# Optimization experiments

Hardware: AMD Instinct MI355X
Metric: run time of the kernel (lower is better)

Reference implementation:

```python
import jax, jax.numpy as jnp
import numpy as np

N = 100000   # nodes
E = 1600000  # edges
IN = 128     # input feature dim
C = 64       # per-layer output dim (filters)
H = 2        # attention heads
EPS = 1e-5   # batchnorm eps


def setup_inputs() -> dict:
    key = jax.random.key(0)
    ks = jax.random.split(key, 32)
    rn = lambda k, s, sc=0.05: jax.random.normal(k, s, jnp.float32) * sc
    inp = {
        "x": jax.random.normal(ks[0], (N, IN), jnp.float32),
        "edge_index": jax.random.randint(ks[1], (2, E), 0, N, jnp.int32),
        # GATConv layer 0 (IN -> C, H heads, concat=False)
        "W0": rn(ks[2], (IN, H * C)), "as0": rn(ks[3], (H, C)), "ad0": rn(ks[4], (H, C)), "b0": jnp.zeros((C,), jnp.float32),
        "skip0": rn(ks[5], (IN, C)),  # Linear(IN->C, bias=False); layers 1,2 skips are Identity
        "g0": jnp.ones((C,), jnp.float32), "be0": jnp.zeros((C,), jnp.float32),
        # GATConv layer 1 (C -> C)
        "W1": rn(ks[6], (C, H * C)), "as1": rn(ks[7], (H, C)), "ad1": rn(ks[8], (H, C)), "b1": jnp.zeros((C,), jnp.float32),
        "g1": jnp.ones((C,), jnp.float32), "be1": jnp.zeros((C,), jnp.float32),
        # GATConv layer 2 (C -> C)
        "W2": rn(ks[9], (C, H * C)), "as2": rn(ks[10], (H, C)), "ad2": rn(ks[11], (H, C)), "b2": jnp.zeros((C,), jnp.float32),
        "g2": jnp.ones((C,), jnp.float32), "be2": jnp.zeros((C,), jnp.float32),
        # JK projection for input (IN -> C, with bias); other projections are Identity
        "projW": rn(ks[12], (IN, C)), "projb": jnp.zeros((C,), jnp.float32),
    }
    return inp


def _gat(x, edge_index, W, a_src, a_dst, b):
    # PyG GATConv, concat=False: mean over heads, bias added after mean.
    h = (x @ W).reshape(-1, H, C)                 # [N, H, C]
    src, dst = edge_index[0], edge_index[1]
    e_src = jnp.sum(h * a_src, axis=-1)           # [N, H]
    e_dst = jnp.sum(h * a_dst, axis=-1)           # [N, H]
    e = jax.nn.leaky_relu(e_src[src] + e_dst[dst], 0.2)  # [E, H]
    m = jax.ops.segment_max(e, dst, num_segments=N)      # neighbor softmax (stable)
    w = jnp.exp(e - m[dst])
    denom = jax.ops.segment_sum(w, dst, num_segments=N)
    alpha = w / (denom[dst] + 1e-16)              # [E, H]
    out = jax.ops.segment_sum(alpha[:, :, None] * h[src], dst, num_segments=N)  # [N, H, C]
    return out.mean(axis=1) + b


def _bn(x, g, b):
    # BatchNorm1d, training-mode batch statistics (deterministic reference)
    mu = x.mean(axis=0)
    var = x.var(axis=0)
    return (x - mu) * jax.lax.rsqrt(var + EPS) * g + b


def reference(x, edge_index, W0, as0, ad0, b0, skip0, g0, be0,
              W1, as1, ad1, b1, g1, be1,
              W2, as2, ad2, b2, g2, be2,
              projW, projb):
    lrelu = lambda v: jax.nn.leaky_relu(v, 0.01)  # nn.LeakyReLU default
    jk0 = x @ projW + projb                       # proj_lyrs[0]
    # layer 0: GAT + projected skip, BN, (dropout=identity in eval), LeakyReLU
    h1 = _gat(x, edge_index, W0, as0, ad0, b0) + x @ skip0
    h1 = lrelu(_bn(h1, g0, be0))
    # layer 1: identity skip
    h2 = _gat(h1, edge_index, W1, as1, ad1, b1) + h1
    h2 = lrelu(_bn(h2, g1, be1))
    # layer 2: identity skip
    h3 = _gat(h2, edge_index, W2, as2, ad2, b2) + h2
    h3 = lrelu(_bn(h3, g2, be2))
    # jumping knowledge, mode='max': elementwise max over [input_proj, h1, h2, h3]
    return jnp.max(jnp.stack([jk0, h1, h2, h3], axis=0), axis=0)
```

## Files before the change

### kernel.cpp

```cpp
#include <hip/hip_runtime.h>

#define NN 100000
#define NE 1600000

constexpr int NBUC = 196;
constexpr int BIN_CHUNK = 4096;
constexpr int NB_BIN = (NE + BIN_CHUNK - 1) / BIN_CHUNK;
constexpr int ACHUNK = 16;

typedef __attribute__((ext_vector_type(8))) short s16x8;
typedef __attribute__((ext_vector_type(4))) float f32x4;
typedef __attribute__((ext_vector_type(2))) float f32x2;

template <int M>
struct IC {
    static constexpr int value = M;
};

__device__ inline unsigned short f2bf(float f) {
    unsigned int u = __float_as_uint(f);
    return (unsigned short)((u + 0x7fffu + ((u >> 16) & 1u)) >> 16);
}
__device__ inline float bf_lo(unsigned int pk) { return __uint_as_float(pk << 16); }
__device__ inline float bf_hi(unsigned int pk) { return __uint_as_float(pk & 0xffff0000u); }
__device__ inline float h2f(unsigned int u) {
    _Float16 h;
    unsigned short s = (unsigned short)u;
    __builtin_memcpy(&h, &s, 2);
    return (float)h;
}

__global__ void zero_u32(unsigned int* p, int n) {
    int i = blockIdx.x * blockDim.x + threadIdx.x;
    if (i < n) p[i] = 0u;
}

__global__ __launch_bounds__(256) void bucket_count(const int* __restrict__ dst,
                                                    int* __restrict__ bcount) {
    __shared__ int hist[NBUC];
    int t = threadIdx.x;
    for (int b = t; b < NBUC; b += 256) hist[b] = 0;
    __syncthreads();
    int beg = blockIdx.x * BIN_CHUNK;
    int end = min(beg + BIN_CHUNK, NE);
    for (int i = beg + t; i < end; i += 256) atomicAdd(&hist[dst[i] >> 9], 1);
    __syncthreads();
    for (int b = t; b < NBUC; b += 256)
        if (hist[b]) atomicAdd(&bcount[b], hist[b]);
}

__global__ void bucket_scan(const int* __restrict__ bcount, int* __restrict__ bbase,
                            int* __restrict__ bucket_cursor, int* __restrict__ offsets) {
    if (threadIdx.x == 0) {
        int run = 0;
        for (int b = 0; b < NBUC; ++b) {
            bbase[b] = run;
            bucket_cursor[b] = run;
            run += bcount[b];
        }
        bbase[NBUC] = NE;
        offsets[NN] = NE;
    }
}

__global__ __launch_bounds__(256) void bin_edges(const int* __restrict__ src,
                                                 const int* __restrict__ dst,
                                                 int* __restrict__ bucket_cursor,
                                                 unsigned int* __restrict__ binned) {
    __shared__ int hist[NBUC];
    __shared__ int base[NBUC];
    int t = threadIdx.x;
    for (int b = t; b < NBUC; b += 256) hist[b] = 0;
    __syncthreads();
    int beg = blockIdx.x * BIN_CHUNK;
    int end = min(beg + BIN_CHUNK, NE);
    for (int i = beg + t; i < end; i += 256) atomicAdd(&hist[dst[i] >> 9], 1);
    __syncthreads();
    for (int b = t; b < NBUC; b += 256) {
        base[b] = hist[b] ? atomicAdd(&bucket_cursor[b], hist[b]) : 0;
        hist[b] = 0;
    }
    __syncthreads();
    for (int i = beg + t; i < end; i += 256) {
        int d = dst[i];
        int bk = d >> 9;
        int loc = atomicAdd(&hist[bk], 1);
        binned[base[bk] + loc] = ((unsigned)(d & 511) << 17) | (unsigned)src[i];
    }
}

__global__ __launch_bounds__(256) void bucket_sort(const unsigned int* __restrict__ binned,
                                                   const int* __restrict__ bbase,
                                                   int* __restrict__ offsets,
                                                   int* __restrict__ csr_src,
                                                   int* __restrict__ csr_dst) {
    __shared__ int deg[512];
    __shared__ int loc[512];
    __shared__ int s2[256];
    int t = threadIdx.x;
    int b = blockIdx.x;
    int beg = bbase[b], end = bbase[b + 1];
    int nbase = b << 9;
    deg[t] = 0;
    deg[t + 256] = 0;
    __syncthreads();
    for (int i = beg + t; i < end; i += 256) atomicAdd(&deg[binned[i] >> 17], 1);
    __syncthreads();
    int pairsum = deg[2 * t] + deg[2 * t + 1];
    s2[t] = pairsum;
    __syncthreads();
    for (int off = 1; off < 256; off <<= 1) {
        int v = (t >= off) ? s2[t - off] : 0;
        __syncthreads();
        s2[t] += v;
        __syncthreads();
    }
    int ex = s2[t] - pairsum;
    loc[2 * t] = ex;
    loc[2 * t + 1] = ex + deg[2 * t];
    __syncthreads();
    for (int i = t; i < 512; i += 256) {
        int node = nbase + i;
        if (node < NN) offsets[node] = beg + loc[i];
    }
    __syncthreads();
    for (int i = beg + t; i < end; i += 256) {
        unsigned int v = binned[i];
        int dl = v >> 17;
        int pos = atomicAdd(&loc[dl], 1);
        csr_src[beg + pos] = (int)(v & 0x1FFFFu);
        csr_dst[beg + pos] = nbase + dl;
    }
}

__global__ void prep_weights(const float* __restrict__ W0, const float* __restrict__ skip0,
                             const float* __restrict__ projW, const float* __restrict__ W1,
                             const float* __restrict__ W2,
                             const float* __restrict__ as0, const float* __restrict__ ad0,
                             const float* __restrict__ as1, const float* __restrict__ ad1,
                             const float* __restrict__ as2, const float* __restrict__ ad2,
                             unsigned short* __restrict__ Wtcat,
                             unsigned short* __restrict__ Wt1,
                             unsigned short* __restrict__ Wt2) {
    int i = blockIdx.x * 256 + threadIdx.x;
    if (i < 16384) {
        int oc = i >> 7, k = i & 127;
        Wtcat[oc * 128 + k] = f2bf(W0[k * 128 + oc]);
    } else if (i < 32768) {
        int j = i - 16384;
        int oc = j >> 7, k = j & 127;
        float v = (oc < 64) ? skip0[k * 64 + oc] : projW[k * 64 + (oc - 64)];
        Wtcat[132 * 128 + oc * 128 + k] = f2bf(v);
    } else if (i < 40960) {
        int j = i - 32768, oc = j >> 6, k = j & 63;
        Wt1[oc * 64 + k] = f2bf(W1[k * 128 + oc]);
    } else if (i < 49152) {
        int j = i - 40960, oc = j >> 6, k = j & 63;
        Wt2[oc * 64 + k] = f2bf(W2[k * 128 + oc]);
    } else if (i < 50688) {
        int e = i - 49152;
        if (e < 512) {
            int k = e >> 2, sc = e & 3, head = sc & 1;
            const float* av = (sc < 2 ? as0 : ad0) + head * 64;
            const float* wr = W0 + k * 128 + head * 64;
            float s = 0.f;
            for (int c = 0; c < 64; ++c) s += wr[c] * av[c];
            Wtcat[(128 + sc) * 128 + k] = f2bf(s);
        } else if (e < 1024) {
            int j = e - 512, k = j >> 2, sc = j & 3;
            Wtcat[132 * 128 + (128 + sc) * 128 + k] = 0;
        } else if (e < 1280) {
            int j = e - 1024, k = j >> 2, sc = j & 3, head = sc & 1;
            const float* av = (sc < 2 ? as1 : ad1) + head * 64;
            const float* wr = W1 + k * 128 + head * 64;
            float s = 0.f;
            for (int c = 0; c < 64; ++c) s += wr[c] * av[c];
            Wt1[(128 + sc) * 64 + k] = f2bf(s);
        } else {
            int j = e - 1280, k = j >> 2, sc = j & 3, head = sc & 1;
            const float* av = (sc < 2 ? as2 : ad2) + head * 64;
            const float* wr = W2 + k * 128 + head * 64;
            float s = 0.f;
            for (int c = 0; c < 64; ++c) s += wr[c] * av[c];
            Wt2[(128 + sc) * 64 + k] = f2bf(s);
        }
    }
}

template <int K, bool L0, bool XFORM>
__global__ __launch_bounds__(256, 4) void gemm_mfma(
    const void* __restrict__ Xv, const unsigned short* __restrict__ Wt,
    unsigned int* __restrict__ Hq32, _Float16* __restrict__ skipx,
    _Float16* __restrict__ jkproj, const float* __restrict__ projb,
    const float* __restrict__ bnsc,
    unsigned int* __restrict__ e_srcpk, unsigned int* __restrict__ e_dstpk) {
    constexpr int KP = K + 8;
    constexpr int NC = 132;
    __shared__ unsigned short Bs[NC * KP];
    int t = threadIdx.x;
    int tile = L0 ? blockIdx.x : 0;
    int rbase = (L0 ? blockIdx.y : blockIdx.x) * 64;
    const unsigned short* Wtg = Wt + (size_t)tile * NC * K;

    for (int i = t; i < NC * (K / 8); i += 256) {
        int oc = i / (K / 8);
        int k8 = (i % (K / 8)) * 8;
        uint4 v = *(const uint4*)&Wtg[(size_t)oc * K + k8];
        *(uint4*)&Bs[oc * KP + k8] = v;
    }

    int lane = t & 63, wv = t >> 6;
    int lr = lane & 15, quad = lane >> 4;
    int arow = wv * 16 + lr;
    int grow = rbase + arow;
    bool rowok = grow < NN;

    s16x8 afrag[K / 32];
#pragma unroll
    for (int ks = 0; ks < K / 32; ++ks) {
        int kq = ks * 32 + quad * 8;
        float v[8];
        if (rowok) {
            if constexpr (!XFORM) {
                const float* Xf = (const float*)Xv;
                float4 p0 = *(const float4*)&Xf[(size_t)grow * K + kq];
                float4 p1 = *(const float4*)&Xf[(size_t)grow * K + kq + 4];
                v[0] = p0.x; v[1] = p0.y; v[2] = p0.z; v[3] = p0.w;
                v[4] = p1.x; v[5] = p1.y; v[6] = p1.z; v[7] = p1.w;
            } else {
                const _Float16* Xh = (const _Float16*)Xv;
                uint4 rw = *(const uint4*)&Xh[(size_t)grow * K + kq];
                unsigned rr[4] = {rw.x, rw.y, rw.z, rw.w};
#pragma unroll
                for (int q = 0; q < 4; ++q) {
                    v[2 * q] = h2f(rr[q]);
                    v[2 * q + 1] = h2f(rr[q] >> 16);
                }
#pragma unroll
                for (int c = 0; c < 8; ++c) {
                    float val = v[c] * bnsc[kq + c] + bnsc[64 + kq + c];
                    v[c] = val >= 0.f ? val : 0.01f * val;
                }
            }
        } else {
#pragma unroll
            for (int c = 0; c < 8; ++c) v[c] = 0.f;
        }
        unsigned short* ap = (unsigned short*)&afrag[ks];
#pragma unroll
        for (int c = 0; c < 8; ++c) ap[c] = f2bf(v[c]);
    }
    __syncthreads();

    f32x4 acc[8];
    f32x4 acc8 = (f32x4)(0.f);
#pragma unroll
    for (int c = 0; c < 8; ++c) acc[c] = (f32x4)(0.f);
#pragma unroll
    for (int ks = 0; ks < K / 32; ++ks) {
        s16x8 a = afrag[ks];
        int k0 = ks * 32;
#pragma unroll
        for (int ct = 0; ct < 8; ++ct) {
            s16x8 b = *(const s16x8*)&Bs[(ct * 16 + lr) * KP + k0 + quad * 8];
            acc[ct] = __builtin_amdgcn_mfma_f32_16x16x32_bf16(a, b, acc[ct], 0, 0, 0);
        }
        s16x8 b9 = *(const s16x8*)&Bs[(128 + (lr & 3)) * KP + k0 + quad * 8];
        acc8 = __builtin_amdgcn_mfma_f32_16x16x32_bf16(a, b9, acc8, 0, 0, 0);
    }

    bool hblock = (!L0) || (tile == 0);
#pragma unroll
    for (int reg = 0; reg < 4; ++reg) {
        int row = rbase + wv * 16 + quad * 4 + reg;
        if (hblock) {
            if (row < NN) {
#pragma unroll
                for (int ct = 0; ct < 4; ++ct) {
                    int pk = __builtin_amdgcn_cvt_pk_fp8_f32(acc[ct][reg], acc[ct + 4][reg],
                                                             0, false);
                    int pn = __shfl_xor(pk, 1, 64);
                    if (!(lr & 1))
                        Hq32[(size_t)row * 32 + ct * 8 + (lr >> 1)] =
                            (unsigned int)((pk & 0xFFFF) | (pn << 16));
                }
            }
            float own = acc8[reg];
            float par = __shfl_xor(own, 1, 64);
            if (row < NN) {
                unsigned int pkv = (unsigned)f2bf(own) | ((unsigned)f2bf(par) << 16);
                if (lr == 0) e_srcpk[row] = pkv;
                else if (lr == 2) e_dstpk[row] = pkv;
            }
        } else if (row < NN) {
#pragma unroll
            for (int ct = 0; ct < 4; ++ct)
                skipx[(size_t)row * 64 + ct * 16 + lr] = (_Float16)acc[ct][reg];
#pragma unroll
            for (int ct = 4; ct < 8; ++ct) {
                int c = (ct - 4) * 16 + lr;
                jkproj[(size_t)row * 64 + c] = (_Float16)(acc[ct][reg] + projb[c]);
            }
        }
    }
}

__global__ void edge_w(const int* __restrict__ csr_src, const int* __restrict__ csr_dst,
                       const unsigned int* __restrict__ e_srcpk,
                       const unsigned int* __restrict__ e_dstpk,
                       uint2* __restrict__ erec) {
    int i = blockIdx.x * blockDim.x + threadIdx.x;
    if (i >= NE) return;
    int s = csr_src[i];
    unsigned int q = e_srcpk[s];
    unsigned int r = e_dstpk[csr_dst[i]];
    float a0 = bf_lo(q) + bf_lo(r);
    float a1 = bf_hi(q) + bf_hi(r);
    a0 = a0 >= 0.f ? a0 : 0.2f * a0;
    a1 = a1 >= 0.f ? a1 : 0.2f * a1;
    unsigned int w = (unsigned int)f2bf(__expf(a0)) | ((unsigned int)f2bf(__expf(a1)) << 16);
    erec[i] = make_uint2((unsigned)s, w);
}

__global__ __launch_bounds__(256) void aggregate(
    const int* __restrict__ offsets, const uint2* __restrict__ erec,
    const unsigned int* __restrict__ Hq32, const _Float16* __restrict__ skipsrc,
    const float* __restrict__ bnsc, const float* __restrict__ bias,
    _Float16* __restrict__ hraw) {
    int wave = threadIdx.x >> 6;
    int lane = threadIdx.x & 63;
    int w = blockIdx.x * 4 + wave;
    int n0 = w * ACHUNK;
    if (n0 >= NN) return;
    int n1 = min(n0 + ACHUNK, NN);
    const unsigned char* __restrict__ Hq8 = (const unsigned char*)Hq32;
    int voff = lane * 2;

    float bsc = 0.f, bsh = 0.f;
    if (bnsc) {
        bsc = bnsc[lane];
        bsh = bnsc[64 + lane];
    }
    float bi = bias[lane];

    int end = __builtin_amdgcn_readfirstlane(offsets[n0]);
    for (int n = n0; n < n1; ++n) {
        int beg = end;
        end = __builtin_amdgcn_readfirstlane(offsets[n + 1]);
        float a0 = 0.f, a1 = 0.f, den0 = 0.f, den1 = 0.f;
        int j = beg;

        auto batch = [&](auto Mc) {
            constexpr int M = decltype(Mc)::value;
            uint2 ee[M];
#pragma unroll
            for (int u = 0; u < M; ++u) ee[u] = erec[j + u];
            int ss[M];
            unsigned ww[M];
#pragma unroll
            for (int u = 0; u < M; ++u) {
                ss[u] = __builtin_amdgcn_readfirstlane((int)ee[u].x);
                ww[u] = (unsigned)__builtin_amdgcn_readfirstlane((int)ee[u].y);
            }
            unsigned short uu[M];
#pragma unroll
            for (int u = 0; u < M; ++u)
                uu[u] = *(const unsigned short*)(Hq8 + (size_t)ss[u] * 128 + voff);
#pragma unroll
            for (int u = 0; u < M; ++u) {
                float w0 = bf_lo(ww[u]), w1 = bf_hi(ww[u]);
                f32x2 hv = __builtin_amdgcn_cvt_pk_f32_fp8((int)uu[u], false);
                den0 += w0;
                den1 += w1;
                a0 += w0 * hv[0];
                a1 += w1 * hv[1];
            }
            j += M;
        };

        while (j + 16 <= end) batch(IC<16>{});
        if (j + 8 <= end) batch(IC<8>{});
        if (j + 4 <= end) batch(IC<4>{});
        if (j + 2 <= end) batch(IC<2>{});
        if (j < end) batch(IC<1>{});

        float sv = (float)skipsrc[(size_t)n * 64 + lane];
        if (bnsc) {
            sv = sv * bsc + bsh;
            sv = sv >= 0.f ? sv : 0.01f * sv;
        }
        float id0 = 1.f / (den0 + 1e-16f), id1 = 1.f / (den1 + 1e-16f);
        float o = 0.5f * (a0 * id0 + a1 * id1) + bi + sv;
        hraw[(size_t)n * 64 + lane] = (_Float16)o;
    }
}

__global__ void bn_stats(const _Float16* __restrict__ x, float* __restrict__ sums) {
    __shared__ float ls[256], ls2[256];
    int t = threadIdx.x;
    int c = t & 63, q = t >> 6;
    float s = 0.f, s2 = 0.f;
    int rbeg = blockIdx.x * 512;
    for (int r = rbeg + q; r < rbeg + 512; r += 4) {
        if (r < NN) {
            float v = (float)x[(size_t)r * 64 + c];
            s += v;
            s2 += v * v;
        }
    }
    ls[t] = s;
    ls2[t] = s2;
    __syncthreads();
    if (t < 64) {
        s = ls[t] + ls[t + 64] + ls[t + 128] + ls[t + 192];
        s2 = ls2[t] + ls2[t + 64] + ls2[t + 128] + ls2[t + 192];
        atomicAdd(&sums[c], s);
        atomicAdd(&sums[64 + c], s2);
    }
}

__global__ void bn_final(const float* __restrict__ sums, const float* __restrict__ g,
                         const float* __restrict__ be, float* __restrict__ sc_sh) {
    int c = threadIdx.x;
    if (c < 64) {
        float mu = sums[c] / (float)NN;
        float var = sums[64 + c] / (float)NN - mu * mu;
        float sc = g[c] * rsqrtf(var + 1e-5f);
        sc_sh[c] = sc;
        sc_sh[64 + c] = be[c] - mu * sc;
    }
}

__global__ void final_out(const _Float16* __restrict__ jkproj, const _Float16* __restrict__ hA,
                          const _Float16* __restrict__ hB, const _Float16* __restrict__ hC,
                          const float* __restrict__ bnAll, float* __restrict__ out) {
    int i = blockIdx.x * blockDim.x + threadIdx.x;
    if (i < NN * 64) {
        int c = i & 63;
        float v0 = (float)hA[i] * bnAll[c] + bnAll[64 + c];
        float v1 = (float)hB[i] * bnAll[128 + c] + bnAll[192 + c];
        float v2 = (float)hC[i] * bnAll[256 + c] + bnAll[320 + c];
        v0 = v0 >= 0.f ? v0 : 0.01f * v0;
        v1 = v1 >= 0.f ? v1 : 0.01f * v1;
        v2 = v2 >= 0.f ? v2 : 0.01f * v2;
        out[i] = fmaxf(fmaxf((float)jkproj[i], v0), fmaxf(v1, v2));
    }
}

extern "C" void kernel_launch(void* const* d_in, const int* in_sizes, int n_in,
                              void* d_out, int out_size, void* d_ws, size_t ws_size,
                              hipStream_t stream) {
    const float* x = (const float*)d_in[0];
    const int* ei = (const int*)d_in[1];
    const int* e_src_idx = ei;
    const int* e_dst_idx = ei + NE;
    const float* W0 = (const float*)d_in[2];
    const float* as0 = (const float*)d_in[3];
    const float* ad0 = (const float*)d_in[4];
    const float* b0 = (const float*)d_in[5];
    const float* skip0 = (const float*)d_in[6];
    const float* g0 = (const float*)d_in[7];
    const float* be0 = (const float*)d_in[8];
    const float* W1 = (const float*)d_in[9];
    const float* as1 = (const float*)d_in[10];
    const float* ad1 = (const float*)d_in[11];
    const float* b1 = (const float*)d_in[12];
    const float* g1 = (const float*)d_in[13];
    const float* be1 = (const float*)d_in[14];
    const float* W2 = (const float*)d_in[15];
    const float* as2 = (const float*)d_in[16];
    const float* ad2 = (const float*)d_in[17];
    const float* b2 = (const float*)d_in[18];
    const float* g2 = (const float*)d_in[19];
    const float* be2 = (const float*)d_in[20];
    const float* projW = (const float*)d_in[21];
    const float* projb = (const float*)d_in[22];
    float* out = (float*)d_out;

    char* p = (char*)d_ws;
    auto alloc = [&](size_t bytes) {
        char* r = p;
        p += (bytes + 255) & ~(size_t)255;
        return r;
    };
    int* zbuf = (int*)alloc((size_t)(196 + 384) * 4);
    int* bcount = zbuf;
    float* bnsumAll = (float*)(zbuf + 196);
    int* bbase = (int*)alloc((size_t)(NBUC + 1) * 4);
    int* bucket_cursor = (int*)alloc((size_t)NBUC * 4);
    int* offsets = (int*)alloc((size_t)(NN + 1) * 4);
    int* csr_src = (int*)alloc((size_t)NE * 4);
    int* csr_dst = (int*)alloc((size_t)NE * 4);
    uint2* erec = (uint2*)alloc((size_t)NE * 8);
    unsigned int* binned = (unsigned int*)alloc((size_t)NE * 4);
    unsigned int* h_q32 = (unsigned int*)alloc((size_t)NN * 32 * 4);
    unsigned int* e_srcpk = (unsigned int*)alloc((size_t)NN * 4);
    unsigned int* e_dstpk = (unsigned int*)alloc((size_t)NN * 4);
    _Float16* skipx = (_Float16*)alloc((size_t)NN * 64 * 2);
    _Float16* jkproj = (_Float16*)alloc((size_t)NN * 64 * 2);
    _Float16* hrawA = (_Float16*)alloc((size_t)NN * 64 * 2);
    _Float16* hrawB = (_Float16*)alloc((size_t)NN * 64 * 2);
    _Float16* hrawC = (_Float16*)alloc((size_t)NN * 64 * 2);
    unsigned short* Wtcat = (unsigned short*)alloc((size_t)2 * 132 * 128 * 2);
    unsigned short* Wt1 = (unsigned short*)alloc((size_t)132 * 64 * 2);
    unsigned short* Wt2 = (unsigned short*)alloc((size_t)132 * 64 * 2);
    float* bnscAll = (float*)alloc(3 * 128 * 4);
    if ((size_t)(p - (char*)d_ws) > ws_size) return;

    zero_u32<<<3, 256, 0, stream>>>((unsigned int*)zbuf, 196 + 384);
    bucket_count<<<NB_BIN, 256, 0, stream>>>(e_dst_idx, bcount);
    bucket_scan<<<1, 64, 0, stream>>>(bcount, bbase, bucket_cursor, offsets);
    bin_edges<<<NB_BIN, 256, 0, stream>>>(e_src_idx, e_dst_idx, bucket_cursor, binned);
    bucket_sort<<<NBUC, 256, 0, stream>>>(binned, bbase, offsets, csr_src, csr_dst);
    prep_weights<<<198, 256, 0, stream>>>(W0, skip0, projW, W1, W2, as0, ad0, as1, ad1,
                                          as2, ad2, Wtcat, Wt1, Wt2);

    int gblocks = (NN + 63) / 64;
    int ablocks = (NN + ACHUNK * 4 - 1) / (ACHUNK * 4);

    gemm_mfma<128, true, false><<<dim3(2, gblocks), 256, 0, stream>>>(
        x, Wtcat, h_q32, skipx, jkproj, projb, nullptr, e_srcpk, e_dstpk);
    edge_w<<<(NE + 255) / 256, 256, 0, stream>>>(csr_src, csr_dst, e_srcpk, e_dstpk, erec);
    aggregate<<<ablocks, 256, 0, stream>>>(offsets, erec, h_q32, skipx, nullptr, b0,
                                           hrawA);
    bn_stats<<<(NN + 511) / 512, 256, 0, stream>>>(hrawA, bnsumAll);
    bn_final<<<1, 64, 0, stream>>>(bnsumAll, g0, be0, bnscAll);

    gemm_mfma<64, false, true><<<dim3(gblocks, 1), 256, 0, stream>>>(
        hrawA, Wt1, h_q32, nullptr, nullptr, nullptr, bnscAll, e_srcpk, e_dstpk);
    edge_w<<<(NE + 255) / 256, 256, 0, stream>>>(csr_src, csr_dst, e_srcpk, e_dstpk, erec);
    aggregate<<<ablocks, 256, 0, stream>>>(offsets, erec, h_q32, hrawA, bnscAll, b1,
                                           hrawB);
    bn_stats<<<(NN + 511) / 512, 256, 0, stream>>>(hrawB, bnsumAll + 128);
    bn_final<<<1, 64, 0, stream>>>(bnsumAll + 128, g1, be1, bnscAll + 128);

    gemm_mfma<64, false, true><<<dim3(gblocks, 1), 256, 0, stream>>>(
        hrawB, Wt2, h_q32, nullptr, nullptr, nullptr, bnscAll + 128, e_srcpk, e_dstpk);
    edge_w<<<(NE + 255) / 256, 256, 0, stream>>>(csr_src, csr_dst, e_srcpk, e_dstpk, erec);
    aggregate<<<ablocks, 256, 0, stream>>>(offsets, erec, h_q32, hrawB, bnscAll + 128,
                                           b2, hrawC);
    bn_stats<<<(NN + 511) / 512, 256, 0, stream>>>(hrawC, bnsumAll + 256);
    bn_final<<<1, 64, 0, stream>>>(bnsumAll + 256, g2, be2, bnscAll + 256);

    final_out<<<(NN * 64 + 255) / 256, 256, 0, stream>>>(jkproj, hrawA, hrawB, hrawC,
                                                         bnscAll, out);
}
```

Baseline: 573.4 us.

## Software-pipeline edge aggregation across node boundaries with triple-buffered record loads

Replaces the per-node batched gather loop with a flat stream over all edges of a wave's node chunk. Edge records are prefetched three chunks ahead and feature gathers one chunk ahead, with node outputs flushed when the edge index crosses a node boundary. The chunk per wave also drops from 16 to 8 nodes. This hides gather latency for low-degree nodes and removes the per-node tail batches, at the cost of more registers, per-edge boundary checks and more complex control flow.

```diff
diff --git a/kernel.cpp b/kernel.cpp
--- a/kernel.cpp
+++ b/kernel.cpp
@@ -6,16 +6,12 @@
 constexpr int NBUC = 196;
 constexpr int BIN_CHUNK = 4096;
 constexpr int NB_BIN = (NE + BIN_CHUNK - 1) / BIN_CHUNK;
-constexpr int ACHUNK = 16;
+constexpr int ACHUNK = 8;
+constexpr int CH = 8;
 
 typedef __attribute__((ext_vector_type(8))) short s16x8;
 typedef __attribute__((ext_vector_type(4))) float f32x4;
 typedef __attribute__((ext_vector_type(2))) float f32x2;
-
-template <int M>
-struct IC {
-    static constexpr int value = M;
-};
 
 __device__ inline unsigned short f2bf(float f) {
     unsigned int u = __float_as_uint(f);
@@ -343,56 +339,95 @@
     }
     float bi = bias[lane];
 
-    int end = __builtin_amdgcn_readfirstlane(offsets[n0]);
-    for (int n = n0; n < n1; ++n) {
-        int beg = end;
-        end = __builtin_amdgcn_readfirstlane(offsets[n + 1]);
-        float a0 = 0.f, a1 = 0.f, den0 = 0.f, den1 = 0.f;
-        int j = beg;
-
-        auto batch = [&](auto Mc) {
-            constexpr int M = decltype(Mc)::value;
-            uint2 ee[M];
-#pragma unroll
-            for (int u = 0; u < M; ++u) ee[u] = erec[j + u];
-            int ss[M];
-            unsigned ww[M];
-#pragma unroll
-            for (int u = 0; u < M; ++u) {
-                ss[u] = __builtin_amdgcn_readfirstlane((int)ee[u].x);
-                ww[u] = (unsigned)__builtin_amdgcn_readfirstlane((int)ee[u].y);
-            }
-            unsigned short uu[M];
-#pragma unroll
-            for (int u = 0; u < M; ++u)
-                uu[u] = *(const unsigned short*)(Hq8 + (size_t)ss[u] * 128 + voff);
-#pragma unroll
-            for (int u = 0; u < M; ++u) {
-                float w0 = bf_lo(ww[u]), w1 = bf_hi(ww[u]);
+    int r0 = __builtin_amdgcn_readfirstlane(offsets[n0]);
+    int r1 = __builtin_amdgcn_readfirstlane(offsets[n1]);
+
+    int curN = n0;
+    int curEnd = __builtin_amdgcn_readfirstlane(offsets[n0 + 1]);
+    int nid = n0 + 2 > n1 ? n1 : n0 + 2;
+    int endNext = __builtin_amdgcn_readfirstlane(offsets[nid]);
+    float sv = (float)skipsrc[(size_t)curN * 64 + lane];
+    float svN = (curN + 1 < n1) ? (float)skipsrc[(size_t)(curN + 1) * 64 + lane] : 0.f;
+
+    float a0 = 0.f, a1 = 0.f, d0 = 0.f, d1 = 0.f;
+
+    auto flush = [&]() {
+        float svv = sv;
+        if (bnsc) {
+            svv = svv * bsc + bsh;
+            svv = svv >= 0.f ? svv : 0.01f * svv;
+        }
+        float id0 = 1.f / (d0 + 1e-16f), id1 = 1.f / (d1 + 1e-16f);
+        float o = 0.5f * (a0 * id0 + a1 * id1) + bi + svv;
+        hraw[(size_t)curN * 64 + lane] = (_Float16)o;
+        a0 = a1 = d0 = d1 = 0.f;
+        ++curN;
+        sv = svN;
+        curEnd = endNext;
+        if (curN + 1 < n1) svN = (float)skipsrc[(size_t)(curN + 1) * 64 + lane];
+        int ni = curN + 2 > n1 ? n1 : curN + 2;
+        endNext = __builtin_amdgcn_readfirstlane(offsets[ni]);
+    };
+
+    uint2 e0[CH], e1[CH], e2[CH];
+    unsigned short u0[CH], u1[CH];
+    int jb = r0;
+
+    auto loadE = [&](uint2 (&ee)[CH], int base) {
+#pragma unroll
+        for (int u = 0; u < CH; ++u) {
+            int idx = base + u;
+            idx = idx < r1 ? idx : r1 - 1;
+            ee[u] = erec[idx];
+        }
+    };
+    auto gath = [&](unsigned short (&uu)[CH], uint2 (&ee)[CH]) {
+#pragma unroll
+        for (int u = 0; u < CH; ++u) {
+            unsigned s = (unsigned)__builtin_amdgcn_readfirstlane((int)ee[u].x);
+            uu[u] = *(const unsigned short*)(Hq8 + (size_t)s * 128 + voff);
+        }
+    };
+    auto consume = [&](unsigned short (&uu)[CH], uint2 (&ee)[CH], int base) {
+#pragma unroll
+        for (int u = 0; u < CH; ++u) {
+            int j = base + u;
+            if (j < r1) {
+                while (j == curEnd && curN < n1) flush();
+                unsigned wwu = (unsigned)__builtin_amdgcn_readfirstlane((int)ee[u].y);
+                float w0 = bf_lo(wwu), w1 = bf_hi(wwu);
                 f32x2 hv = __builtin_amdgcn_cvt_pk_f32_fp8((int)uu[u], false);
-                den0 += w0;
-                den1 += w1;
+                d0 += w0;
+                d1 += w1;
                 a0 += w0 * hv[0];
                 a1 += w1 * hv[1];
             }
-            j += M;
-        };
-
-        while (j + 16 <= end) batch(IC<16>{});
-        if (j + 8 <= end) batch(IC<8>{});
-        if (j + 4 <= end) batch(IC<4>{});
-        if (j + 2 <= end) batch(IC<2>{});
-        if (j < end) batch(IC<1>{});
-
-        float sv = (float)skipsrc[(size_t)n * 64 + lane];
-        if (bnsc) {
-            sv = sv * bsc + bsh;
-            sv = sv >= 0.f ? sv : 0.01f * sv;
-        }
-        float id0 = 1.f / (den0 + 1e-16f), id1 = 1.f / (den1 + 1e-16f);
-        float o = 0.5f * (a0 * id0 + a1 * id1) + bi + sv;
-        hraw[(size_t)n * 64 + lane] = (_Float16)o;
-    }
+        }
+    };
+
+#define AG_STEP(UI, EI, UC, EC, EL)            \
+    if (jb + CH < r1) gath(UI, EI);            \
+    consume(UC, EC, jb);                       \
+    if (jb + 3 * CH < r1) loadE(EL, jb + 3 * CH); \
+    jb += CH;                                  \
+    if (jb >= r1) break;
+
+    if (r1 > r0) {
+        loadE(e0, r0);
+        if (r0 + CH < r1) loadE(e1, r0 + CH);
+        if (r0 + 2 * CH < r1) loadE(e2, r0 + 2 * CH);
+        gath(u0, e0);
+        for (;;) {
+            AG_STEP(u1, e1, u0, e0, e0)
+            AG_STEP(u0, e2, u1, e1, e1)
+            AG_STEP(u1, e0, u0, e2, e2)
+            AG_STEP(u0, e1, u1, e0, e0)
+            AG_STEP(u1, e2, u0, e1, e1)
+            AG_STEP(u0, e0, u1, e2, e2)
+        }
+    }
+#undef AG_STEP
+    while (curN < n1) flush();
 }
 
 __global__ void bn_stats(const _Float16* __restrict__ x, float* __restrict__ sums) {
```

After: 654.1 us. 1.14x slower.
